# Kernel tuning notes

Hardware: AMD Instinct MI355X
Metric: run time of the kernel (lower is better)

The kernel has to match this reference:

```python
import jax, jax.numpy as jnp
import numpy as np

B, NS, NT = 4, 512, 512
D_IN, C1, R, C2 = 128, 64, 32, 32
E = 32768
STEPS = 10


def setup_inputs() -> dict:
    key = jax.random.key(0)
    ks = jax.random.split(key, 12)
    inp = {}
    inp['x_s'] = jax.random.normal(ks[0], (B * NS, D_IN), jnp.float32)
    inp['edge_index_s'] = jax.random.randint(ks[1], (2, E), 0, B * NS, jnp.int32)
    inp['edge_attr_s'] = jax.random.uniform(ks[2], (E,), jnp.float32)
    inp['batch_s'] = (jnp.arange(B * NS, dtype=jnp.int32) // NS)
    inp['x_t'] = jax.random.normal(ks[3], (B * NT, D_IN), jnp.float32)
    inp['edge_index_t'] = jax.random.randint(ks[4], (2, E), 0, B * NT, jnp.int32)
    inp['edge_attr_t'] = jax.random.uniform(ks[5], (E,), jnp.float32)
    inp['batch_t'] = (jnp.arange(B * NT, dtype=jnp.int32) // NT)
    inp['W1'] = jax.random.normal(ks[6], (D_IN, C1), jnp.float32) / np.float32(np.sqrt(D_IN))
    inp['W2'] = jax.random.normal(ks[7], (R, C2), jnp.float32) / np.float32(np.sqrt(R))
    inp['mw1'] = jax.random.normal(ks[8], (C2, C2), jnp.float32) / np.float32(np.sqrt(C2))
    inp['mb1'] = jnp.zeros((C2,), jnp.float32)
    inp['mw2'] = jax.random.normal(ks[9], (C2, 1), jnp.float32) / np.float32(np.sqrt(C2))
    inp['mb2'] = jnp.zeros((1,), jnp.float32)
    inp['r'] = jax.random.normal(ks[10], (STEPS, B, NS, R), jnp.float32)
    return inp


def psi(x, src, dst, ea, W, n):
    # simple message-passing GNN: edge-weighted neighbor aggregation + linear + ReLU
    m = jax.ops.segment_sum(x[src] * ea[:, None], dst, num_segments=n)
    return jax.nn.relu((x + m) @ W)


def reference(x_s, edge_index_s, edge_attr_s, batch_s, x_t, edge_index_t, edge_attr_t,
              batch_t, W1, W2, mw1, mb1, mw2, mb2, r):
    # Uniform graph sizes -> to_dense_batch is a reshape and all masks are True,
    # so masked_softmax reduces to plain softmax; batch_s/batch_t kept for interface fidelity.
    ss, ds = edge_index_s[0], edge_index_s[1]
    st, dt = edge_index_t[0], edge_index_t[1]
    h_s = psi(x_s, ss, ds, edge_attr_s, W1, B * NS).reshape(B, NS, C1)
    h_t = psi(x_t, st, dt, edge_attr_t, W1, B * NT).reshape(B, NT, C1)
    S_hat0 = jnp.einsum('bsc,btc->bst', h_s, h_t)  # [B, NS, NT]
    S_0 = jax.nn.softmax(S_hat0, axis=-1)

    def step(S_hat, r_i):
        S = jax.nn.softmax(S_hat, axis=-1)
        r_t = jnp.einsum('bst,bsr->btr', S, r_i)  # S^T @ r_s
        o_s = psi(r_i.reshape(B * NS, R), ss, ds, edge_attr_s, W2, B * NS).reshape(B, NS, C2)
        o_t = psi(r_t.reshape(B * NT, R), st, dt, edge_attr_t, W2, B * NT).reshape(B, NT, C2)
        Dm = o_s[:, :, None, :] - o_t[:, None, :, :]  # [B, NS, NT, C2] outer difference
        upd = (jax.nn.relu(Dm @ mw1 + mb1) @ mw2 + mb2)[..., 0]
        return S_hat + upd, None

    S_hat, _ = jax.lax.scan(step, S_hat0, r)
    S_L = jax.nn.softmax(S_hat, axis=-1)
    return (S_0, S_L)
```

## Files before the change

kernel.cpp:

```cpp
#include <hip/hip_runtime.h>


constexpr int kB = 4;
constexpr int kNS = 512;
constexpr int kNT = 512;
constexpr int kDin = 128;
constexpr int kC1 = 64;
constexpr int kR = 32;
constexpr int kC2 = 32;
constexpr int kE = 32768;
constexpr int kSteps = 10;
constexpr int kN = kB * kNS;
constexpr int kChunkStride = kR * kN;

__global__ void k_hist(const int* __restrict__ ei_s, const int* __restrict__ ei_t,
                       int* __restrict__ deg) {
  int g = blockIdx.y;
  const int* dst = (g ? ei_t : ei_s) + kE;
  int e = blockIdx.x * 256 + threadIdx.x;
  atomicAdd(&deg[g * kN + dst[e]], 1);
}

__global__ void k_scan(const int* __restrict__ deg, int* __restrict__ off,
                       int* __restrict__ cur) {
  int g = blockIdx.x;
  const int* d = deg + g * kN;
  int* o = off + g * (kN + 1);
  int* c = cur + g * kN;
  __shared__ int sums[256];
  int tid = threadIdx.x;
  int loc[8];
  int s = 0;
#pragma unroll
  for (int i = 0; i < 8; ++i) { loc[i] = d[tid * 8 + i]; s += loc[i]; }
  sums[tid] = s;
  __syncthreads();
  for (int st = 1; st < 256; st <<= 1) {
    int v = (tid >= st) ? sums[tid - st] : 0;
    __syncthreads();
    sums[tid] += v;
    __syncthreads();
  }
  int base = (tid > 0) ? sums[tid - 1] : 0;
#pragma unroll
  for (int i = 0; i < 8; ++i) {
    int idx = tid * 8 + i;
    o[idx] = base;
    c[idx] = base;
    base += loc[i];
  }
  if (tid == 255) o[kN] = base;
}

__global__ void k_scatter(const int* __restrict__ ei_s, const int* __restrict__ ei_t,
                          const float* __restrict__ ea_s, const float* __restrict__ ea_t,
                          int* __restrict__ cur, int* __restrict__ srcs,
                          float* __restrict__ eaw) {
  int g = blockIdx.y;
  const int* ei = g ? ei_t : ei_s;
  const float* ea = g ? ea_t : ea_s;
  int e = blockIdx.x * 256 + threadIdx.x;
  int d = ei[kE + e];
  int srcv = ei[e];
  int pos = atomicAdd(&cur[g * kN + d], 1);
  srcs[g * kE + pos] = srcv;
  eaw[g * kE + pos] = ea[e];
}

__global__ __launch_bounds__(128) void k_psi1(
    const float* __restrict__ x_s, const float* __restrict__ x_t,
    const int* __restrict__ srcs, const float* __restrict__ eaw,
    const int* __restrict__ off, const float* __restrict__ W1, float* __restrict__ h) {
  int g = blockIdx.y;
  const float* x = g ? x_t : x_s;
  const int* sr = srcs + g * kE;
  const float* ew = eaw + g * kE;
  const int* o = off + g * (kN + 1);
  float* ho = h + (size_t)g * kN * kC1;
  int n = blockIdx.x, f = threadIdx.x;
  __shared__ float y[kDin];
  int beg = o[n], end = o[n + 1];
  float m = 0.f;
  for (int idx = beg; idx < end; ++idx)
    m += x[(size_t)sr[idx] * kDin + f] * ew[idx];
  y[f] = x[(size_t)n * kDin + f] + m;
  __syncthreads();
  if (f < kC1) {
    float acc = 0.f;
#pragma unroll 16
    for (int k = 0; k < kDin; ++k) acc += y[k] * W1[k * kC1 + f];
    ho[(size_t)n * kC1 + f] = fmaxf(acc, 0.f);
  }
}

__global__ __launch_bounds__(256) void k_shat0(const float* __restrict__ h,
                                               float* __restrict__ Shat) {
  int b = blockIdx.z, s0 = blockIdx.y * 64, t0 = blockIdx.x * 64;
  const float* hs = h + (size_t)(b * kNS + s0) * kC1;
  const float* ht = h + (size_t)kN * kC1 + (size_t)(b * kNT + t0) * kC1;
  __shared__ float As[64 * 68];
  __shared__ float Bs[64 * 68];
  int tid = threadIdx.x;
#pragma unroll
  for (int k2 = 0; k2 < 4; ++k2) {
    int idx = tid + k2 * 256;
    int row = idx >> 4, c4 = idx & 15;
    float4 va = *(const float4*)(hs + (size_t)row * kC1 + c4 * 4);
    *(float4*)&As[row * 68 + c4 * 4] = va;
    float4 vb = *(const float4*)(ht + (size_t)row * kC1 + c4 * 4);
    *(float4*)&Bs[row * 68 + c4 * 4] = vb;
  }
  __syncthreads();
  int ts = tid >> 4, tt = tid & 15;
  float acc[4][4] = {};
#pragma unroll
  for (int cc = 0; cc < 16; ++cc) {
    float4 a[4], bt[4];
#pragma unroll
    for (int i = 0; i < 4; ++i) a[i] = *(const float4*)&As[(ts * 4 + i) * 68 + cc * 4];
#pragma unroll
    for (int k = 0; k < 4; ++k) bt[k] = *(const float4*)&Bs[(tt + 16 * k) * 68 + cc * 4];
#pragma unroll
    for (int i = 0; i < 4; ++i)
#pragma unroll
      for (int k = 0; k < 4; ++k)
        acc[i][k] += a[i].x * bt[k].x + a[i].y * bt[k].y + a[i].z * bt[k].z + a[i].w * bt[k].w;
  }
#pragma unroll
  for (int i = 0; i < 4; ++i) {
    int s = s0 + ts * 4 + i;
    float* row = Shat + (size_t)(b * kNS + s) * kNT;
#pragma unroll
    for (int k = 0; k < 4; ++k) row[t0 + tt + 16 * k] = acc[i][k];
  }
}

__global__ __launch_bounds__(256) void k_softmax(const float* __restrict__ Shat,
                                                 float* __restrict__ dst,
                                                 float* __restrict__ pstatm,
                                                 float* __restrict__ pstatl) {
  int row = blockIdx.x, tid = threadIdx.x;
  const float* p = Shat + (size_t)row * kNT;
  float v0 = p[tid], v1 = p[tid + 256];
  __shared__ float sm[4];
  float mx = fmaxf(v0, v1);
#pragma unroll
  for (int o = 32; o; o >>= 1) mx = fmaxf(mx, __shfl_down(mx, o, 64));
  if ((tid & 63) == 0) sm[tid >> 6] = mx;
  __syncthreads();
  mx = fmaxf(fmaxf(sm[0], sm[1]), fmaxf(sm[2], sm[3]));
  float e0 = __expf(v0 - mx), e1 = __expf(v1 - mx);
  float s = e0 + e1;
  __syncthreads();
#pragma unroll
  for (int o = 32; o; o >>= 1) s += __shfl_down(s, o, 64);
  if ((tid & 63) == 0) sm[tid >> 6] = s;
  __syncthreads();
  float tot = sm[0] + sm[1] + sm[2] + sm[3];
  float rinv = 1.f / tot;
  if (tid == 0) {
    pstatm[row] = mx;
    pstatl[row] = tot;
    pstatm[kN + row] = -3.4e38f;
    pstatl[kN + row] = 0.f;
  }
  float* d = dst + (size_t)row * kNT;
  d[tid] = e0 * rinv;
  d[tid + 256] = e1 * rinv;
}

__global__ __launch_bounds__(256) void k_rt(const float* __restrict__ Shat,
                                            const float* __restrict__ pstatm,
                                            const float* __restrict__ pstatl,
                                            const float* __restrict__ ri,
                                            float* __restrict__ part) {
  int b = blockIdx.z, cs = blockIdx.y, s0 = cs * 64, t0 = blockIdx.x * 64;
  __shared__ float Wt[64 * 64];
  __shared__ float rch[64 * 32];
  __shared__ float lm[64], ll[64];
  int tid = threadIdx.x;
  if (tid < 64) {
    int row = b * kNS + s0 + tid;
    float m0 = pstatm[row], m1 = pstatm[kN + row];
    float l0 = pstatl[row], l1 = pstatl[kN + row];
    float m = fmaxf(m0, m1);
    lm[tid] = m;
    ll[tid] = 1.f / (__expf(m0 - m) * l0 + __expf(m1 - m) * l1);
  }
  __syncthreads();
#pragma unroll
  for (int k2 = 0; k2 < 4; ++k2) {
    int idx = tid + k2 * 256;
    int row = idx >> 4, c4 = idx & 15;
    int grow = b * kNS + s0 + row;
    float4 v = *(const float4*)(Shat + (size_t)grow * kNT + t0 + c4 * 4);
    float m = lm[row], l = ll[row];
    float4 wv;
    wv.x = __expf(v.x - m) * l;
    wv.y = __expf(v.y - m) * l;
    wv.z = __expf(v.z - m) * l;
    wv.w = __expf(v.w - m) * l;
    *(float4*)&Wt[row * 64 + c4 * 4] = wv;
  }
#pragma unroll
  for (int k2 = 0; k2 < 2; ++k2) {
    int idx = tid + k2 * 256;
    int row = idx >> 3, c4 = idx & 7;
    float4 v = *(const float4*)(ri + (size_t)(b * kNS + s0 + row) * kR + c4 * 4);
    *(float4*)&rch[row * 32 + c4 * 4] = v;
  }
  __syncthreads();
  int t_l = tid & 63, jg = tid >> 6;
  float acc[8] = {};
  for (int s = 0; s < 64; ++s) {
    float wv = Wt[s * 64 + t_l];
    float4 ra = *(const float4*)&rch[s * 32 + jg * 8];
    float4 rb = *(const float4*)&rch[s * 32 + jg * 8 + 4];
    acc[0] += wv * ra.x; acc[1] += wv * ra.y; acc[2] += wv * ra.z; acc[3] += wv * ra.w;
    acc[4] += wv * rb.x; acc[5] += wv * rb.y; acc[6] += wv * rb.z; acc[7] += wv * rb.w;
  }
  int gcol = b * kNT + t0 + t_l;
  float* dst = part + (size_t)cs * kChunkStride + (size_t)jg * 8 * kN + gcol;
#pragma unroll
  for (int q = 0; q < 8; ++q) dst[(size_t)q * kN] = acc[q];
}

__global__ __launch_bounds__(256) void k_red(const float* __restrict__ part,
                                             float* __restrict__ rt) {
  int idx = blockIdx.x * 256 + threadIdx.x;
  int j = idx >> 11, col = idx & (kN - 1);
  float s = 0.f;
#pragma unroll
  for (int cs = 0; cs < 8; ++cs) s += part[(size_t)cs * kChunkStride + idx];
  rt[(size_t)col * kR + j] = s;
}

__device__ __forceinline__ void psi2_node(
    int n, const float* __restrict__ vin, const int* __restrict__ sr,
    const float* __restrict__ ew, const int* __restrict__ o,
    const float* __restrict__ W2, const float* __restrict__ mw1,
    const float* __restrict__ mb1, float* __restrict__ Pout) {
  int lane = threadIdx.x & 63;
  int f = lane & 31, hh = lane >> 5;
  int beg = o[n], end = o[n + 1];
  float m = 0.f;
  for (int idx = beg + hh; idx < end; idx += 2)
    m += vin[(size_t)sr[idx] * kR + f] * ew[idx];
  m += __shfl_down(m, 32, 64);
  float v = vin[(size_t)n * kR + f] + m;
  float acc = 0.f;
#pragma unroll
  for (int k = 0; k < kC2; ++k) acc += __shfl(v, k, 64) * W2[k * kC2 + f];
  float ov = fmaxf(acc, 0.f);
  float p = mb1 ? mb1[f] : 0.f;
#pragma unroll
  for (int k = 0; k < kC2; ++k) p += __shfl(ov, k, 64) * mw1[k * kC2 + f];
  if (lane < 32) Pout[(size_t)n * kC2 + f] = p;
}

__global__ __launch_bounds__(256) void k_psi2(
    const float* __restrict__ ri, const float* __restrict__ rtv,
    const int* __restrict__ srcs, const float* __restrict__ eaw,
    const int* __restrict__ off, const float* __restrict__ W2,
    const float* __restrict__ mw1, const float* __restrict__ mb1,
    float* __restrict__ Ps, float* __restrict__ Pt) {
  int n = blockIdx.x * 4 + (threadIdx.x >> 6);
  psi2_node(n, ri, srcs, eaw, off, W2, mw1, mb1, Ps);
  psi2_node(n, rtv, srcs + kE, eaw + kE, off + (kN + 1), W2, mw1, nullptr, Pt);
}

__global__ __launch_bounds__(256) void k_upd(
    float* __restrict__ Shat, const float* __restrict__ Ps,
    const float* __restrict__ Pt, const float* __restrict__ mw2,
    const float* __restrict__ mb2, float* __restrict__ pstatm,
    float* __restrict__ pstatl) {
  __shared__ float pts[256 * 33];
  __shared__ float red[8 * 4];
  __shared__ float lmx[8];
  int tid = threadIdx.x;
  int g0 = blockIdx.x * 8;
  int cc = blockIdx.y;
  int bb = g0 >> 9;
  int c0 = cc * 256;
  const float4* PtB = (const float4*)(Pt + ((size_t)bb * kNT + c0) * kC2);
#pragma unroll
  for (int k = 0; k < 8; ++k) {
    int idx = tid + k * 256;
    int col = idx >> 3, q = idx & 7;
    float4 v = PtB[idx];
    float* d = &pts[col * 33 + q * 4];
    d[0] = v.x; d[1] = v.y; d[2] = v.z; d[3] = v.w;
  }
  __syncthreads();
  float pt[32];
#pragma unroll
  for (int j = 0; j < 32; ++j) pt[j] = pts[tid * 33 + j];
  float bias = mb2[0];
  float nv[8];
#pragma unroll
  for (int s = 0; s < 8; ++s) {
    const float* psr = Ps + (size_t)(g0 + s) * kC2;
    float u = 0.f;
#pragma unroll
    for (int j = 0; j < 32; ++j) u += fmaxf(psr[j] - pt[j], 0.f) * mw2[j];
    float* p = Shat + (size_t)(g0 + s) * kNT + c0 + tid;
    float v = *p + u + bias;
    *p = v;
    nv[s] = v;
  }
  int wv = tid >> 6, ln = tid & 63;
#pragma unroll
  for (int s = 0; s < 8; ++s) {
    float m = nv[s];
#pragma unroll
    for (int o2 = 32; o2; o2 >>= 1) m = fmaxf(m, __shfl_down(m, o2, 64));
    if (ln == 0) red[s * 4 + wv] = m;
  }
  __syncthreads();
  if (tid < 8) {
    lmx[tid] = fmaxf(fmaxf(red[tid * 4], red[tid * 4 + 1]),
                     fmaxf(red[tid * 4 + 2], red[tid * 4 + 3]));
  }
  __syncthreads();
#pragma unroll
  for (int s = 0; s < 8; ++s) {
    float e = __expf(nv[s] - lmx[s]);
#pragma unroll
    for (int o2 = 32; o2; o2 >>= 1) e += __shfl_down(e, o2, 64);
    if (ln == 0) red[s * 4 + wv] = e;
  }
  __syncthreads();
  if (tid < 8) {
    float l = red[tid * 4] + red[tid * 4 + 1] + red[tid * 4 + 2] + red[tid * 4 + 3];
    pstatm[cc * kN + g0 + tid] = lmx[tid];
    pstatl[cc * kN + g0 + tid] = l;
  }
}

extern "C" void kernel_launch(void* const* d_in, const int* in_sizes, int n_in,
                              void* d_out, int out_size, void* d_ws, size_t ws_size,
                              hipStream_t stream) {
  (void)in_sizes; (void)n_in; (void)out_size; (void)ws_size;
  const float* x_s = (const float*)d_in[0];
  const int* ei_s = (const int*)d_in[1];
  const float* ea_s = (const float*)d_in[2];
  const float* x_t = (const float*)d_in[4];
  const int* ei_t = (const int*)d_in[5];
  const float* ea_t = (const float*)d_in[6];
  const float* W1 = (const float*)d_in[8];
  const float* W2 = (const float*)d_in[9];
  const float* mw1 = (const float*)d_in[10];
  const float* mb1 = (const float*)d_in[11];
  const float* mw2 = (const float*)d_in[12];
  const float* mb2 = (const float*)d_in[13];
  const float* r = (const float*)d_in[14];
  float* out = (float*)d_out;

  char* w = (char*)d_ws;
  auto alloc = [&](size_t bytes) -> void* {
    void* p = (void*)w;
    w += (bytes + 255) & ~(size_t)255;
    return p;
  };
  int* deg = (int*)alloc((size_t)2 * kN * 4);
  int* off = (int*)alloc((size_t)2 * (kN + 1) * 4);
  int* cur = (int*)alloc((size_t)2 * kN * 4);
  int* srcs = (int*)alloc((size_t)2 * kE * 4);
  float* eaw = (float*)alloc((size_t)2 * kE * 4);
  float* h = (float*)alloc((size_t)2 * kN * kC1 * 4);
  float* Shat = (float*)alloc((size_t)kB * kNS * kNT * 4);
  float* pstatm = (float*)alloc((size_t)2 * kN * 4);
  float* pstatl = (float*)alloc((size_t)2 * kN * 4);
  float* rt = (float*)alloc((size_t)kN * kR * 4);
  float* Ps = (float*)alloc((size_t)kN * kC2 * 4);
  float* Pt = (float*)alloc((size_t)kN * kC2 * 4);
  float* part = (float*)alloc((size_t)8 * kChunkStride * 4);

  hipMemsetAsync(deg, 0, (size_t)2 * kN * 4, stream);
  k_hist<<<dim3(kE / 256, 2), 256, 0, stream>>>(ei_s, ei_t, deg);
  k_scan<<<2, 256, 0, stream>>>(deg, off, cur);
  k_scatter<<<dim3(kE / 256, 2), 256, 0, stream>>>(ei_s, ei_t, ea_s, ea_t, cur, srcs, eaw);
  k_psi1<<<dim3(kN, 2), 128, 0, stream>>>(x_s, x_t, srcs, eaw, off, W1, h);
  k_shat0<<<dim3(8, 8, kB), 256, 0, stream>>>(h, Shat);
  k_softmax<<<kN, 256, 0, stream>>>(Shat, out, pstatm, pstatl);
  k_rt<<<dim3(8, 8, kB), 256, 0, stream>>>(Shat, pstatm, pstatl, r, part);
  k_red<<<kChunkStride / 256, 256, 0, stream>>>(part, rt);
  for (int i = 0; i < kSteps; ++i) {
    const float* ri = r + (size_t)i * kN * kR;
    k_psi2<<<kN / 4, 256, 0, stream>>>(ri, rt, srcs, eaw, off, W2, mw1, mb1, Ps, Pt);
    k_upd<<<dim3(kN / 8, 2), 256, 0, stream>>>(Shat, Ps, Pt, mw2, mb2, pstatm, pstatl);
    if (i + 1 < kSteps) {
      k_rt<<<dim3(8, 8, kB), 256, 0, stream>>>(Shat, pstatm, pstatl,
                                               ri + (size_t)kN * kR, part);
      k_red<<<kChunkStride / 256, 256, 0, stream>>>(part, rt);
    }
  }
  k_softmax<<<kN, 256, 0, stream>>>(Shat, out + (size_t)kB * kNS * kNT, pstatm, pstatl);
}
```

Baseline: 485.7 us.

## Fuse softmax stats into GEMM, hoist source psi out of loop, drop reduction kernel

```diff
diff --git a/kernel.cpp b/kernel.cpp
--- a/kernel.cpp
+++ b/kernel.cpp
@@ -94,7 +94,9 @@
 }
 
 __global__ __launch_bounds__(256) void k_shat0(const float* __restrict__ h,
-                                               float* __restrict__ Shat) {
+                                               float* __restrict__ Shat,
+                                               float* __restrict__ pstatm,
+                                               float* __restrict__ pstatl) {
   int b = blockIdx.z, s0 = blockIdx.y * 64, t0 = blockIdx.x * 64;
   const float* hs = h + (size_t)(b * kNS + s0) * kC1;
   const float* ht = h + (size_t)kN * kC1 + (size_t)(b * kNT + t0) * kC1;
@@ -133,65 +135,49 @@
 #pragma unroll
     for (int k = 0; k < 4; ++k) row[t0 + tt + 16 * k] = acc[i][k];
   }
-}
-
-__global__ __launch_bounds__(256) void k_softmax(const float* __restrict__ Shat,
-                                                 float* __restrict__ dst,
-                                                 float* __restrict__ pstatm,
-                                                 float* __restrict__ pstatl) {
-  int row = blockIdx.x, tid = threadIdx.x;
-  const float* p = Shat + (size_t)row * kNT;
-  float v0 = p[tid], v1 = p[tid + 256];
-  __shared__ float sm[4];
-  float mx = fmaxf(v0, v1);
-#pragma unroll
-  for (int o = 32; o; o >>= 1) mx = fmaxf(mx, __shfl_down(mx, o, 64));
-  if ((tid & 63) == 0) sm[tid >> 6] = mx;
-  __syncthreads();
-  mx = fmaxf(fmaxf(sm[0], sm[1]), fmaxf(sm[2], sm[3]));
-  float e0 = __expf(v0 - mx), e1 = __expf(v1 - mx);
-  float s = e0 + e1;
-  __syncthreads();
-#pragma unroll
-  for (int o = 32; o; o >>= 1) s += __shfl_down(s, o, 64);
-  if ((tid & 63) == 0) sm[tid >> 6] = s;
-  __syncthreads();
-  float tot = sm[0] + sm[1] + sm[2] + sm[3];
-  float rinv = 1.f / tot;
-  if (tid == 0) {
-    pstatm[row] = mx;
-    pstatl[row] = tot;
-    pstatm[kN + row] = -3.4e38f;
-    pstatl[kN + row] = 0.f;
-  }
-  float* d = dst + (size_t)row * kNT;
-  d[tid] = e0 * rinv;
-  d[tid + 256] = e1 * rinv;
+#pragma unroll
+  for (int i = 0; i < 4; ++i) {
+    float mm = fmaxf(fmaxf(acc[i][0], acc[i][1]), fmaxf(acc[i][2], acc[i][3]));
+#pragma unroll
+    for (int o2 = 8; o2; o2 >>= 1) mm = fmaxf(mm, __shfl_xor(mm, o2, 64));
+    float se = 0.f;
+#pragma unroll
+    for (int k = 0; k < 4; ++k) se += __expf(acc[i][k] - mm);
+#pragma unroll
+    for (int o2 = 8; o2; o2 >>= 1) se += __shfl_xor(se, o2, 64);
+    if (tt == 0) {
+      int grow = b * kNS + s0 + ts * 4 + i;
+      pstatm[blockIdx.x * kN + grow] = mm;
+      pstatl[blockIdx.x * kN + grow] = se;
+    }
+  }
 }
 
 __global__ __launch_bounds__(256) void k_rt(const float* __restrict__ Shat,
                                             const float* __restrict__ pstatm,
                                             const float* __restrict__ pstatl,
                                             const float* __restrict__ ri,
-                                            float* __restrict__ part) {
-  int b = blockIdx.z, cs = blockIdx.y, s0 = cs * 64, t0 = blockIdx.x * 64;
-  __shared__ float Wt[64 * 64];
+                                            float* __restrict__ part, int nc,
+                                            float* __restrict__ Sout) {
+  int b = blockIdx.z, cs = blockIdx.y, s0 = cs * 64, t0 = blockIdx.x * 32;
+  __shared__ float Wt[64 * 32];
   __shared__ float rch[64 * 32];
   __shared__ float lm[64], ll[64];
   int tid = threadIdx.x;
   if (tid < 64) {
     int row = b * kNS + s0 + tid;
-    float m0 = pstatm[row], m1 = pstatm[kN + row];
-    float l0 = pstatl[row], l1 = pstatl[kN + row];
-    float m = fmaxf(m0, m1);
+    float m = -3.4e38f;
+    for (int c = 0; c < nc; ++c) m = fmaxf(m, pstatm[c * kN + row]);
+    float l = 0.f;
+    for (int c = 0; c < nc; ++c) l += __expf(pstatm[c * kN + row] - m) * pstatl[c * kN + row];
     lm[tid] = m;
-    ll[tid] = 1.f / (__expf(m0 - m) * l0 + __expf(m1 - m) * l1);
-  }
-  __syncthreads();
-#pragma unroll
-  for (int k2 = 0; k2 < 4; ++k2) {
+    ll[tid] = 1.f / l;
+  }
+  __syncthreads();
+#pragma unroll
+  for (int k2 = 0; k2 < 2; ++k2) {
     int idx = tid + k2 * 256;
-    int row = idx >> 4, c4 = idx & 15;
+    int row = idx >> 3, c4 = idx & 7;
     int grow = b * kNS + s0 + row;
     float4 v = *(const float4*)(Shat + (size_t)grow * kNT + t0 + c4 * 4);
     float m = lm[row], l = ll[row];
@@ -200,39 +186,21 @@
     wv.y = __expf(v.y - m) * l;
     wv.z = __expf(v.z - m) * l;
     wv.w = __expf(v.w - m) * l;
-    *(float4*)&Wt[row * 64 + c4 * 4] = wv;
-  }
-#pragma unroll
-  for (int k2 = 0; k2 < 2; ++k2) {
-    int idx = tid + k2 * 256;
-    int row = idx >> 3, c4 = idx & 7;
-    float4 v = *(const float4*)(ri + (size_t)(b * kNS + s0 + row) * kR + c4 * 4);
-    *(float4*)&rch[row * 32 + c4 * 4] = v;
-  }
-  __syncthreads();
-  int t_l = tid & 63, jg = tid >> 6;
-  float acc[8] = {};
+    *(float4*)&Wt[row * 32 + c4 * 4] = wv;
+    if (Sout) *(float4*)(Sout + (size_t)grow * kNT + t0 + c4 * 4) = wv;
+    float4 rv = *(const float4*)(ri + (size_t)grow * kR + c4 * 4);
+    *(float4*)&rch[row * 32 + c4 * 4] = rv;
+  }
+  __syncthreads();
+  int t_l = tid & 31, jg = tid >> 5;
+  float4 acc = make_float4(0.f, 0.f, 0.f, 0.f);
   for (int s = 0; s < 64; ++s) {
-    float wv = Wt[s * 64 + t_l];
-    float4 ra = *(const float4*)&rch[s * 32 + jg * 8];
-    float4 rb = *(const float4*)&rch[s * 32 + jg * 8 + 4];
-    acc[0] += wv * ra.x; acc[1] += wv * ra.y; acc[2] += wv * ra.z; acc[3] += wv * ra.w;
-    acc[4] += wv * rb.x; acc[5] += wv * rb.y; acc[6] += wv * rb.z; acc[7] += wv * rb.w;
+    float wv = Wt[s * 32 + t_l];
+    float4 rv = *(const float4*)&rch[s * 32 + jg * 4];
+    acc.x += wv * rv.x; acc.y += wv * rv.y; acc.z += wv * rv.z; acc.w += wv * rv.w;
   }
   int gcol = b * kNT + t0 + t_l;
-  float* dst = part + (size_t)cs * kChunkStride + (size_t)jg * 8 * kN + gcol;
-#pragma unroll
-  for (int q = 0; q < 8; ++q) dst[(size_t)q * kN] = acc[q];
-}
-
-__global__ __launch_bounds__(256) void k_red(const float* __restrict__ part,
-                                             float* __restrict__ rt) {
-  int idx = blockIdx.x * 256 + threadIdx.x;
-  int j = idx >> 11, col = idx & (kN - 1);
-  float s = 0.f;
-#pragma unroll
-  for (int cs = 0; cs < 8; ++cs) s += part[(size_t)cs * kChunkStride + idx];
-  rt[(size_t)col * kR + j] = s;
+  *(float4*)&part[(size_t)cs * kChunkStride + (size_t)gcol * kR + jg * 4] = acc;
 }
 
 __device__ __forceinline__ void psi2_node(
@@ -258,15 +226,50 @@
   if (lane < 32) Pout[(size_t)n * kC2 + f] = p;
 }
 
-__global__ __launch_bounds__(256) void k_psi2(
-    const float* __restrict__ ri, const float* __restrict__ rtv,
-    const int* __restrict__ srcs, const float* __restrict__ eaw,
-    const int* __restrict__ off, const float* __restrict__ W2,
-    const float* __restrict__ mw1, const float* __restrict__ mb1,
-    float* __restrict__ Ps, float* __restrict__ Pt) {
+__global__ __launch_bounds__(256) void k_psi2s(
+    const float* __restrict__ r, const int* __restrict__ srcs,
+    const float* __restrict__ eaw, const int* __restrict__ off,
+    const float* __restrict__ W2, const float* __restrict__ mw1,
+    const float* __restrict__ mb1, float* __restrict__ PsAll) {
+  int nn = blockIdx.x * 4 + (threadIdx.x >> 6);
+  int step = nn >> 11, node = nn & (kN - 1);
+  psi2_node(node, r + (size_t)step * kN * kR, srcs, eaw, off, W2, mw1, mb1,
+            PsAll + (size_t)step * kN * kR);
+}
+
+__global__ __launch_bounds__(256) void k_psi2t(
+    const float* __restrict__ part, const int* __restrict__ srcs,
+    const float* __restrict__ eaw, const int* __restrict__ off,
+    const float* __restrict__ W2, const float* __restrict__ mw1,
+    float* __restrict__ Pt) {
   int n = blockIdx.x * 4 + (threadIdx.x >> 6);
-  psi2_node(n, ri, srcs, eaw, off, W2, mw1, mb1, Ps);
-  psi2_node(n, rtv, srcs + kE, eaw + kE, off + (kN + 1), W2, mw1, nullptr, Pt);
+  int lane = threadIdx.x & 63;
+  int f = lane & 31, hh = lane >> 5;
+  const int* sr = srcs + kE;
+  const float* ew = eaw + kE;
+  const int* o = off + (kN + 1);
+  int beg = o[n], end = o[n + 1];
+  float m = 0.f;
+  for (int idx = beg + hh; idx < end; idx += 2) {
+    int rr = sr[idx];
+    float v = 0.f;
+#pragma unroll
+    for (int cs = 0; cs < 8; ++cs) v += part[(size_t)cs * kChunkStride + (size_t)rr * kR + f];
+    m += v * ew[idx];
+  }
+  m += __shfl_down(m, 32, 64);
+  float vown = 0.f;
+#pragma unroll
+  for (int cs = 0; cs < 8; ++cs) vown += part[(size_t)cs * kChunkStride + (size_t)n * kR + f];
+  float v = vown + m;
+  float acc = 0.f;
+#pragma unroll
+  for (int k = 0; k < kC2; ++k) acc += __shfl(v, k, 64) * W2[k * kC2 + f];
+  float ov = fmaxf(acc, 0.f);
+  float p = 0.f;
+#pragma unroll
+  for (int k = 0; k < kC2; ++k) p += __shfl(ov, k, 64) * mw1[k * kC2 + f];
+  if (lane < 32) Pt[(size_t)n * kC2 + f] = p;
 }
 
 __global__ __launch_bounds__(256) void k_upd(
@@ -335,6 +338,21 @@
     pstatm[cc * kN + g0 + tid] = lmx[tid];
     pstatl[cc * kN + g0 + tid] = l;
   }
+}
+
+__global__ __launch_bounds__(256) void k_out(const float* __restrict__ Shat,
+                                             const float* __restrict__ pstatm,
+                                             const float* __restrict__ pstatl,
+                                             float* __restrict__ out) {
+  int row = blockIdx.x, tid = threadIdx.x;
+  float m0 = pstatm[row], m1 = pstatm[kN + row];
+  float l0 = pstatl[row], l1 = pstatl[kN + row];
+  float m = fmaxf(m0, m1);
+  float linv = 1.f / (__expf(m0 - m) * l0 + __expf(m1 - m) * l1);
+  const float* p = Shat + (size_t)row * kNT;
+  float* d = out + (size_t)row * kNT;
+  d[tid] = __expf(p[tid] - m) * linv;
+  d[tid + 256] = __expf(p[tid + 256] - m) * linv;
 }
 
 extern "C" void kernel_launch(void* const* d_in, const int* in_sizes, int n_in,
@@ -369,10 +387,9 @@
   float* eaw = (float*)alloc((size_t)2 * kE * 4);
   float* h = (float*)alloc((size_t)2 * kN * kC1 * 4);
   float* Shat = (float*)alloc((size_t)kB * kNS * kNT * 4);
-  float* pstatm = (float*)alloc((size_t)2 * kN * 4);
-  float* pstatl = (float*)alloc((size_t)2 * kN * 4);
-  float* rt = (float*)alloc((size_t)kN * kR * 4);
-  float* Ps = (float*)alloc((size_t)kN * kC2 * 4);
+  float* pstatm = (float*)alloc((size_t)8 * kN * 4);
+  float* pstatl = (float*)alloc((size_t)8 * kN * 4);
+  float* PsAll = (float*)alloc((size_t)kSteps * kN * kR * 4);
   float* Pt = (float*)alloc((size_t)kN * kC2 * 4);
   float* part = (float*)alloc((size_t)8 * kChunkStride * 4);
 
@@ -380,20 +397,19 @@
   k_hist<<<dim3(kE / 256, 2), 256, 0, stream>>>(ei_s, ei_t, deg);
   k_scan<<<2, 256, 0, stream>>>(deg, off, cur);
   k_scatter<<<dim3(kE / 256, 2), 256, 0, stream>>>(ei_s, ei_t, ea_s, ea_t, cur, srcs, eaw);
+  k_psi2s<<<kSteps * kN / 4, 256, 0, stream>>>(r, srcs, eaw, off, W2, mw1, mb1, PsAll);
   k_psi1<<<dim3(kN, 2), 128, 0, stream>>>(x_s, x_t, srcs, eaw, off, W1, h);
-  k_shat0<<<dim3(8, 8, kB), 256, 0, stream>>>(h, Shat);
-  k_softmax<<<kN, 256, 0, stream>>>(Shat, out, pstatm, pstatl);
-  k_rt<<<dim3(8, 8, kB), 256, 0, stream>>>(Shat, pstatm, pstatl, r, part);
-  k_red<<<kChunkStride / 256, 256, 0, stream>>>(part, rt);
+  k_shat0<<<dim3(8, 8, kB), 256, 0, stream>>>(h, Shat, pstatm, pstatl);
+  k_rt<<<dim3(16, 8, kB), 256, 0, stream>>>(Shat, pstatm, pstatl, r, part, 8, out);
   for (int i = 0; i < kSteps; ++i) {
-    const float* ri = r + (size_t)i * kN * kR;
-    k_psi2<<<kN / 4, 256, 0, stream>>>(ri, rt, srcs, eaw, off, W2, mw1, mb1, Ps, Pt);
-    k_upd<<<dim3(kN / 8, 2), 256, 0, stream>>>(Shat, Ps, Pt, mw2, mb2, pstatm, pstatl);
+    k_psi2t<<<kN / 4, 256, 0, stream>>>(part, srcs, eaw, off, W2, mw1, Pt);
+    k_upd<<<dim3(kN / 8, 2), 256, 0, stream>>>(Shat, PsAll + (size_t)i * kN * kR, Pt,
+                                               mw2, mb2, pstatm, pstatl);
     if (i + 1 < kSteps) {
-      k_rt<<<dim3(8, 8, kB), 256, 0, stream>>>(Shat, pstatm, pstatl,
-                                               ri + (size_t)kN * kR, part);
-      k_red<<<kChunkStride / 256, 256, 0, stream>>>(part, rt);
+      k_rt<<<dim3(16, 8, kB), 256, 0, stream>>>(Shat, pstatm, pstatl,
+                                                r + (size_t)(i + 1) * kN * kR, part,
+                                                2, nullptr);
     }
   }
-  k_softmax<<<kN, 256, 0, stream>>>(Shat, out + (size_t)kB * kNS * kNT, pstatm, pstatl);
-}
+  k_out<<<kN, 256, 0, stream>>>(Shat, pstatm, pstatl, out + (size_t)kB * kNS * kNT);
+}
```

Result: slower. 523.5 us (+7.8%).
